# Kernel optimization log

Measured on AMD Instinct MI355X. Metric: run time of the kernel, lower is better.

Reference implementation:

```python
import jax, jax.numpy as jnp
import numpy as np

N = 50_000          # nodes
E = 1_600_000       # edges (avg degree 32)
F_IN = 8            # num_static_node_features
F_OUT = 12          # num_timesteps_in (TGCN hidden)
PERIODS = 6         # num_timesteps_out


def setup_inputs() -> dict:
    key = jax.random.key(0)
    ks = jax.random.split(key, 12)
    def n(k, shape, s=0.2):
        return jax.random.normal(k, shape, jnp.float32) * s
    return {
        "x": jax.random.normal(ks[0], (N, F_IN, PERIODS), jnp.float32),
        "edge_index": jax.random.randint(ks[1], (2, E), 0, N, dtype=jnp.int32),
        "edge_weight": jax.random.uniform(ks[2], (E,), jnp.float32),
        "att": n(ks[3], (PERIODS,), 1.0),
        "Wz": n(ks[4], (F_IN, F_OUT)), "bz": jnp.zeros((F_OUT,), jnp.float32),
        "Wr": n(ks[5], (F_IN, F_OUT)), "br": jnp.zeros((F_OUT,), jnp.float32),
        "Wh": n(ks[6], (F_IN, F_OUT)), "bh": jnp.zeros((F_OUT,), jnp.float32),
        "lzW": n(ks[7], (F_OUT, 2 * F_OUT)), "lzb": jnp.zeros((F_OUT,), jnp.float32),
        "lrW": n(ks[8], (F_OUT, 2 * F_OUT)), "lrb": jnp.zeros((F_OUT,), jnp.float32),
        "lhW": n(ks[9], (F_OUT, 2 * F_OUT)), "lhb": jnp.zeros((F_OUT,), jnp.float32),
        "linW": n(ks[10], (PERIODS, F_OUT)), "linb": jnp.zeros((PERIODS,), jnp.float32),
    }


def _gcn_norm(edge_index, edge_weight):
    # PyG gcn_norm: add self loops (weight 1.0), symmetric D^-1/2 A D^-1/2,
    # degree computed from dst (col) of edge_weight.
    src, dst = edge_index[0], edge_index[1]
    loop = jnp.arange(N, dtype=src.dtype)
    src = jnp.concatenate([src, loop])
    dst = jnp.concatenate([dst, loop])
    ew = jnp.concatenate([edge_weight, jnp.ones((N,), edge_weight.dtype)])
    deg = jax.ops.segment_sum(ew, dst, num_segments=N)
    dinv = jnp.where(deg > 0, 1.0 / jnp.sqrt(deg), 0.0)
    return src, dst, dinv[src] * ew * dinv[dst]


def _gcn_conv(xp, W, b, src, dst, norm):
    h = xp @ W                                  # [N, F_OUT]
    msg = norm[:, None] * h[src]                # gather over edges
    return jax.ops.segment_sum(msg, dst, num_segments=N) + b


def reference(x, edge_index, edge_weight, att, Wz, bz, Wr, br, Wh, bh,
              lzW, lzb, lrW, lrb, lhW, lhb, linW, linb):
    src, dst, norm = _gcn_norm(edge_index, edge_weight)
    H0 = jnp.zeros((N, F_OUT), x.dtype)  # A3TGCN passes H=None each period

    def tgcn_cell(xp):  # xp: [N, F_IN]
        Z = jax.nn.sigmoid(
            jnp.concatenate([_gcn_conv(xp, Wz, bz, src, dst, norm), H0], -1) @ lzW.T + lzb)
        R = jax.nn.sigmoid(
            jnp.concatenate([_gcn_conv(xp, Wr, br, src, dst, norm), H0], -1) @ lrW.T + lrb)
        Ht = jnp.tanh(
            jnp.concatenate([_gcn_conv(xp, Wh, bh, src, dst, norm), H0 * R], -1) @ lhW.T + lhb)
        return Z * H0 + (1.0 - Z) * Ht

    probs = jax.nn.softmax(att)                  # [P]
    Hs = jax.vmap(tgcn_cell, in_axes=2)(x)       # [P, N, F_OUT]
    H = jnp.einsum('p,pnf->nf', probs, Hs)       # attention-weighted sum
    h = jax.nn.relu(H)
    return h @ linW.T + linb                     # [N, PERIODS]
```

## Files before the change

kernel.cpp:

```cpp
#include <hip/hip_runtime.h>
#include <hip/hip_fp16.h>

#define N_NODES 50000
#define N_EDGES 1600000
#define F_IN 8
#define F_OUT 12
#define PERIODS 6
#define FP 48
#define BKT_SH 7
#define BKT_N 128
#define NBKT ((N_NODES + BKT_N - 1) / BKT_N)
#define CHK 2048
#define NCHK ((N_EDGES + CHK - 1) / CHK)
#define SEG_CAP 4736
#define SRC_MASK 0x1FFFFu

__global__ void __launch_bounds__(256) k_hist(const int* __restrict__ dst,
                                              unsigned int* __restrict__ hist) {
    __shared__ unsigned int h[NBKT];
    int tid = threadIdx.x, blk = blockIdx.x;
    for (int k = tid; k < NBKT; k += 256) h[k] = 0u;
    __syncthreads();
    int base = blk * CHK;
    for (int i = tid; i < CHK; i += 256) {
        int e = base + i;
        if (e < N_EDGES) atomicAdd(&h[dst[e] >> BKT_SH], 1u);
    }
    __syncthreads();
    for (int k = tid; k < NBKT; k += 256) hist[(size_t)blk * NBKT + k] = h[k];
}

__global__ void __launch_bounds__(1024) k_colscan(unsigned int* __restrict__ hist,
                                                  unsigned int* __restrict__ tot) {
    __shared__ unsigned int arr[1024];
    int t = threadIdx.x, k = blockIdx.x;
    unsigned int v = (t < NCHK) ? hist[(size_t)t * NBKT + k] : 0u;
    arr[t] = v;
    __syncthreads();
    for (int off = 1; off < 1024; off <<= 1) {
        unsigned int u = (t >= off) ? arr[t - off] : 0u;
        __syncthreads();
        arr[t] += u;
        __syncthreads();
    }
    if (t < NCHK) hist[(size_t)t * NBKT + k] = arr[t] - v;
    if (t == NCHK - 1) tot[k] = arr[t];
}

__global__ void __launch_bounds__(512) k_scatter(const int* __restrict__ src,
                                                 const int* __restrict__ dst,
                                                 const float* __restrict__ ew,
                                                 const unsigned int* __restrict__ colpre,
                                                 const unsigned int* __restrict__ tot,
                                                 unsigned long long* __restrict__ part) {
    __shared__ unsigned int arr[512];
    __shared__ unsigned int ldsOff[NBKT];
    int tid = threadIdx.x, blk = blockIdx.x;
    unsigned int v = (tid < NBKT) ? tot[tid] : 0u;
    arr[tid] = v;
    __syncthreads();
    for (int off = 1; off < 512; off <<= 1) {
        unsigned int u = (tid >= off) ? arr[tid - off] : 0u;
        __syncthreads();
        arr[tid] += u;
        __syncthreads();
    }
    if (tid < NBKT)
        ldsOff[tid] = (arr[tid] - v) + colpre[(size_t)blk * NBKT + tid];
    __syncthreads();
    int base = blk * CHK;
    for (int i = tid; i < CHK; i += 512) {
        int e = base + i;
        if (e >= N_EDGES) continue;
        int s = src[e], d = dst[e];
        unsigned int pos = atomicAdd(&ldsOff[d >> BKT_SH], 1u);
        unsigned int lo = ((unsigned int)(d & (BKT_N - 1)) << 24) | (unsigned int)s;
        part[pos] = ((unsigned long long)__float_as_uint(ew[e]) << 32) | lo;
    }
}

__global__ void __launch_bounds__(512) k_bucket(unsigned long long* __restrict__ part,
                                                const unsigned int* __restrict__ tot,
                                                const float* __restrict__ x,
                                                int* __restrict__ offs,
                                                float* __restrict__ dinv_g,
                                                uint2* __restrict__ xs) {
    __shared__ uint2 stage[SEG_CAP];
    __shared__ unsigned int arr[512];
    __shared__ unsigned int cnt[BKT_N], cnt2[BKT_N], rowstart[BKT_N], sc[BKT_N];
    __shared__ float degf[BKT_N], dinv_l[BKT_N];
    int tid = threadIdx.x, k = blockIdx.x;
    unsigned int v = (tid < NBKT) ? tot[tid] : 0u;
    arr[tid] = v;
    __syncthreads();
    for (int off = 1; off < 512; off <<= 1) {
        unsigned int u = (tid >= off) ? arr[tid - off] : 0u;
        __syncthreads();
        arr[tid] += u;
        __syncthreads();
    }
    unsigned int base = (k > 0) ? arr[k - 1] : 0u;
    unsigned int m = tot[k];
    if (m > SEG_CAP) m = SEG_CAP;
    if (tid < BKT_N) { cnt[tid] = 0u; cnt2[tid] = 0u; degf[tid] = 1.0f; }
    __syncthreads();
    for (unsigned int i = tid; i < m; i += 512) {
        unsigned long long p = part[base + i];
        unsigned int lo = (unsigned int)p;
        unsigned int hi = (unsigned int)(p >> 32);
        stage[i] = make_uint2(lo, hi);
        unsigned int j = (lo >> 24) & (BKT_N - 1);
        atomicAdd(&cnt[j], 1u);
        atomicAdd(&degf[j], __uint_as_float(hi));
    }
    __syncthreads();
    if (tid < BKT_N) sc[tid] = cnt[tid];
    __syncthreads();
    for (int off = 1; off < BKT_N; off <<= 1) {
        unsigned int u = (tid >= (unsigned)off && tid < BKT_N) ? sc[tid - off] : 0u;
        __syncthreads();
        if (tid < BKT_N) sc[tid] += u;
        __syncthreads();
    }
    if (tid < BKT_N) rowstart[tid] = sc[tid] - cnt[tid];
    __syncthreads();

    int n0 = k * BKT_N;
    int nn = N_NODES - n0; if (nn > BKT_N) nn = BKT_N;

    if (tid < BKT_N) {
        float dv = rsqrtf(degf[tid]);
        dinv_l[tid] = dv;
        if (tid < nn) {
            dinv_g[n0 + tid] = dv;
            offs[n0 + tid] = (int)(base + rowstart[tid]);
        }
    }
    if (k == NBKT - 1 && tid == 0) offs[N_NODES] = N_EDGES;

    for (unsigned int i = tid; i < m; i += 512) {
        uint2 vv = stage[i];
        unsigned int j = (vv.x >> 24) & (BKT_N - 1);
        unsigned int r = atomicAdd(&cnt2[j], 1u);
        part[base + rowstart[j] + r] = ((unsigned long long)vv.y << 32) | vv.x;
    }
    __syncthreads();

    for (int idx = tid; idx < nn * 12; idx += 512) {
        int j = idx / 12, c = idx % 12;
        int n = n0 + j;
        float di = dinv_l[j];
        const float4* xr = (const float4*)(x + (size_t)n * FP + c * 4);
        float4 a = xr[0];
        __half2 h0 = __floats2half2_rn(di * a.x, di * a.y);
        __half2 h1 = __floats2half2_rn(di * a.z, di * a.w);
        uint2 o;
        o.x = *(unsigned int*)&h0; o.y = *(unsigned int*)&h1;
        xs[(size_t)n * 12 + c] = o;
    }
}

__global__ void __launch_bounds__(256) k_gather(const uint2* __restrict__ xs,
                                                const float* __restrict__ dinv,
                                                const int* __restrict__ offs,
                                                const unsigned long long* __restrict__ part,
                                                uint2* __restrict__ xagg2) {
    int t = blockIdx.x * 256 + threadIdx.x;
    if (t >= N_NODES * 12) return;
    int n = t / 12, c = t % 12;
    uint2 self = xs[(size_t)n * 12 + c];
    float2 f0 = __half22float2(*(__half2*)&self.x);
    float2 f1 = __half22float2(*(__half2*)&self.y);
    float a0 = f0.x, a1 = f0.y, a2 = f1.x, a3 = f1.y;
    int b = offs[n], e = offs[n + 1];
    int kk = b;
    for (; kk + 8 <= e; kk += 8) {
        unsigned long long p[8];
        uint2 v[8];
        #pragma unroll
        for (int u = 0; u < 8; u++) p[u] = part[kk + u];
        #pragma unroll
        for (int u = 0; u < 8; u++)
            v[u] = xs[(size_t)((unsigned int)p[u] & SRC_MASK) * 12 + c];
        #pragma unroll
        for (int u = 0; u < 8; u++) {
            float w = __uint_as_float((unsigned int)(p[u] >> 32));
            float2 e0 = __half22float2(*(__half2*)&v[u].x);
            float2 e1 = __half22float2(*(__half2*)&v[u].y);
            a0 += w * e0.x; a1 += w * e0.y; a2 += w * e1.x; a3 += w * e1.y;
        }
    }
    for (; kk + 4 <= e; kk += 4) {
        unsigned long long p[4];
        uint2 v[4];
        #pragma unroll
        for (int u = 0; u < 4; u++) p[u] = part[kk + u];
        #pragma unroll
        for (int u = 0; u < 4; u++)
            v[u] = xs[(size_t)((unsigned int)p[u] & SRC_MASK) * 12 + c];
        #pragma unroll
        for (int u = 0; u < 4; u++) {
            float w = __uint_as_float((unsigned int)(p[u] >> 32));
            float2 e0 = __half22float2(*(__half2*)&v[u].x);
            float2 e1 = __half22float2(*(__half2*)&v[u].y);
            a0 += w * e0.x; a1 += w * e0.y; a2 += w * e1.x; a3 += w * e1.y;
        }
    }
    for (; kk < e; kk++) {
        unsigned long long p = part[kk];
        float w = __uint_as_float((unsigned int)(p >> 32));
        uint2 v = xs[(size_t)((unsigned int)p & SRC_MASK) * 12 + c];
        float2 e0 = __half22float2(*(__half2*)&v.x);
        float2 e1 = __half22float2(*(__half2*)&v.y);
        a0 += w * e0.x; a1 += w * e0.y; a2 += w * e1.x; a3 += w * e1.y;
    }
    float di = dinv[n];
    __half2 o0 = __floats2half2_rn(di * a0, di * a1);
    __half2 o1 = __floats2half2_rn(di * a2, di * a3);
    uint2 o;
    o.x = *(unsigned int*)&o0; o.y = *(unsigned int*)&o1;
    xagg2[(size_t)n * 12 + c] = o;
}

__global__ void k_node(const uint2* __restrict__ xagg2, const float* __restrict__ att,
                       const float* __restrict__ Wz, const float* __restrict__ bz,
                       const float* __restrict__ Wh, const float* __restrict__ bh,
                       const float* __restrict__ lzW, const float* __restrict__ lzb,
                       const float* __restrict__ lhW, const float* __restrict__ lhb,
                       const float* __restrict__ linW, const float* __restrict__ linb,
                       float* __restrict__ out) {
    int n = blockIdx.x * blockDim.x + threadIdx.x;
    if (n >= N_NODES) return;

    float a[PERIODS];
    float m = -1e30f;
    #pragma unroll
    for (int p = 0; p < PERIODS; p++) { a[p] = att[p]; m = fmaxf(m, a[p]); }
    float se = 0.f;
    #pragma unroll
    for (int p = 0; p < PERIODS; p++) { a[p] = __expf(a[p] - m); se += a[p]; }
    float inv = 1.f / se;
    #pragma unroll
    for (int p = 0; p < PERIODS; p++) a[p] *= inv;

    float row[FP];
    const uint2* xr = xagg2 + (size_t)n * 12;
    #pragma unroll
    for (int i = 0; i < 12; i++) {
        uint2 v = xr[i];
        float2 f0 = __half22float2(*(__half2*)&v.x);
        float2 f1 = __half22float2(*(__half2*)&v.y);
        row[4 * i] = f0.x; row[4 * i + 1] = f0.y;
        row[4 * i + 2] = f1.x; row[4 * i + 3] = f1.y;
    }

    float H[F_OUT];
    #pragma unroll
    for (int j = 0; j < F_OUT; j++) H[j] = 0.f;

    for (int p = 0; p < PERIODS; p++) {
        float gz[F_OUT], gh[F_OUT];
        #pragma unroll
        for (int j = 0; j < F_OUT; j++) { gz[j] = bz[j]; gh[j] = bh[j]; }
        #pragma unroll
        for (int f = 0; f < F_IN; f++) {
            float xv = row[f * PERIODS + p];
            #pragma unroll
            for (int j = 0; j < F_OUT; j++) {
                gz[j] += xv * Wz[f * F_OUT + j];
                gh[j] += xv * Wh[f * F_OUT + j];
            }
        }
        #pragma unroll
        for (int j = 0; j < F_OUT; j++) {
            float z = lzb[j], t2 = lhb[j];
            #pragma unroll
            for (int kk = 0; kk < F_OUT; kk++) {
                z  += gz[kk] * lzW[j * (2 * F_OUT) + kk];
                t2 += gh[kk] * lhW[j * (2 * F_OUT) + kk];
            }
            float Z = 1.f / (1.f + __expf(-z));
            H[j] += a[p] * (1.f - Z) * tanhf(t2);
        }
    }

    float* op = out + (size_t)n * PERIODS;
    #pragma unroll
    for (int q = 0; q < PERIODS; q++) {
        float acc = linb[q];
        #pragma unroll
        for (int j = 0; j < F_OUT; j++)
            acc += fmaxf(H[j], 0.f) * linW[q * F_OUT + j];
        op[q] = acc;
    }
}

extern "C" void kernel_launch(void* const* d_in, const int* in_sizes, int n_in,
                              void* d_out, int out_size, void* d_ws, size_t ws_size,
                              hipStream_t stream) {
    const float* x    = (const float*)d_in[0];
    const int*   ei   = (const int*)d_in[1];
    const float* ew   = (const float*)d_in[2];
    const float* att  = (const float*)d_in[3];
    const float* Wz   = (const float*)d_in[4];
    const float* bz   = (const float*)d_in[5];
    const float* Wh   = (const float*)d_in[8];
    const float* bh   = (const float*)d_in[9];
    const float* lzW  = (const float*)d_in[10];
    const float* lzb  = (const float*)d_in[11];
    const float* lhW  = (const float*)d_in[14];
    const float* lhb  = (const float*)d_in[15];
    const float* linW = (const float*)d_in[16];
    const float* linb = (const float*)d_in[17];
    float* out = (float*)d_out;

    unsigned long long* part = (unsigned long long*)d_ws;
    uint2* xs = (uint2*)(part + N_EDGES);
    uint2* xagg2 = xs + (size_t)N_NODES * 12;
    unsigned int* hist = (unsigned int*)(xagg2 + (size_t)N_NODES * 12);
    float* dinv = (float*)(hist + (size_t)NCHK * NBKT);
    int*   offs = (int*)(dinv + N_NODES);
    unsigned int* tot = (unsigned int*)(offs + N_NODES + 1);

    const int* srcp = ei;
    const int* dstp = ei + N_EDGES;

    k_hist<<<NCHK, 256, 0, stream>>>(dstp, hist);
    k_colscan<<<NBKT, 1024, 0, stream>>>(hist, tot);
    k_scatter<<<NCHK, 512, 0, stream>>>(srcp, dstp, ew, hist, tot, part);
    k_bucket<<<NBKT, 512, 0, stream>>>(part, tot, x, offs, dinv, xs);
    k_gather<<<(N_NODES * 12 + 255) / 256, 256, 0, stream>>>(xs, dinv, offs, part, xagg2);
    k_node<<<(N_NODES + 255) / 256, 256, 0, stream>>>(xagg2, att, Wz, bz, Wh, bh,
                                                      lzW, lzb, lhW, lhb, linW, linb, out);
}
```

Before: 220.4 us.

## Replace histogram+scan bucketing with fixed-capacity buckets and atomic cursors

Removes the separate histogram and column-scan kernels. Each bucket now gets a fixed SEG_CAP slot region, and k_scatter claims per-block offsets with one global atomicAdd per bucket on a cursor array. Node offsets become int2 (begin, end) pairs because rows are no longer contiguous across buckets. This saves two kernel launches and a pass over dst, but it drops edges if any bucket overflows SEG_CAP and makes edge order within a bucket nondeterministic.

```diff
diff --git a/kernel.cpp b/kernel.cpp
--- a/kernel.cpp
+++ b/kernel.cpp
@@ -15,92 +15,64 @@
 #define SEG_CAP 4736
 #define SRC_MASK 0x1FFFFu
 
-__global__ void __launch_bounds__(256) k_hist(const int* __restrict__ dst,
-                                              unsigned int* __restrict__ hist) {
-    __shared__ unsigned int h[NBKT];
-    int tid = threadIdx.x, blk = blockIdx.x;
-    for (int k = tid; k < NBKT; k += 256) h[k] = 0u;
-    __syncthreads();
-    int base = blk * CHK;
-    for (int i = tid; i < CHK; i += 256) {
-        int e = base + i;
-        if (e < N_EDGES) atomicAdd(&h[dst[e] >> BKT_SH], 1u);
-    }
-    __syncthreads();
-    for (int k = tid; k < NBKT; k += 256) hist[(size_t)blk * NBKT + k] = h[k];
-}
-
-__global__ void __launch_bounds__(1024) k_colscan(unsigned int* __restrict__ hist,
-                                                  unsigned int* __restrict__ tot) {
-    __shared__ unsigned int arr[1024];
-    int t = threadIdx.x, k = blockIdx.x;
-    unsigned int v = (t < NCHK) ? hist[(size_t)t * NBKT + k] : 0u;
-    arr[t] = v;
-    __syncthreads();
-    for (int off = 1; off < 1024; off <<= 1) {
-        unsigned int u = (t >= off) ? arr[t - off] : 0u;
-        __syncthreads();
-        arr[t] += u;
-        __syncthreads();
-    }
-    if (t < NCHK) hist[(size_t)t * NBKT + k] = arr[t] - v;
-    if (t == NCHK - 1) tot[k] = arr[t];
+__global__ void k_zero(unsigned int* __restrict__ cursor) {
+    int i = threadIdx.x;
+    if (i < NBKT) cursor[i] = 0u;
 }
 
 __global__ void __launch_bounds__(512) k_scatter(const int* __restrict__ src,
                                                  const int* __restrict__ dst,
                                                  const float* __restrict__ ew,
-                                                 const unsigned int* __restrict__ colpre,
-                                                 const unsigned int* __restrict__ tot,
+                                                 unsigned int* __restrict__ cursor,
                                                  unsigned long long* __restrict__ part) {
-    __shared__ unsigned int arr[512];
-    __shared__ unsigned int ldsOff[NBKT];
+    __shared__ unsigned int h[NBKT];
+    __shared__ unsigned int gbase[NBKT];
     int tid = threadIdx.x, blk = blockIdx.x;
-    unsigned int v = (tid < NBKT) ? tot[tid] : 0u;
-    arr[tid] = v;
-    __syncthreads();
-    for (int off = 1; off < 512; off <<= 1) {
-        unsigned int u = (tid >= off) ? arr[tid - off] : 0u;
-        __syncthreads();
-        arr[tid] += u;
-        __syncthreads();
-    }
-    if (tid < NBKT)
-        ldsOff[tid] = (arr[tid] - v) + colpre[(size_t)blk * NBKT + tid];
+    for (int k = tid; k < NBKT; k += 512) h[k] = 0u;
     __syncthreads();
     int base = blk * CHK;
-    for (int i = tid; i < CHK; i += 512) {
-        int e = base + i;
-        if (e >= N_EDGES) continue;
-        int s = src[e], d = dst[e];
-        unsigned int pos = atomicAdd(&ldsOff[d >> BKT_SH], 1u);
-        unsigned int lo = ((unsigned int)(d & (BKT_N - 1)) << 24) | (unsigned int)s;
-        part[pos] = ((unsigned long long)__float_as_uint(ew[e]) << 32) | lo;
+    int bv[4]; unsigned int lr[4], lo[4], hiw[4]; bool val[4];
+    #pragma unroll
+    for (int u = 0; u < 4; u++) {
+        int e = base + u * 512 + tid;
+        val[u] = (e < N_EDGES);
+        if (val[u]) {
+            int s = src[e], d = dst[e];
+            int b = d >> BKT_SH;
+            bv[u] = b;
+            lr[u] = atomicAdd(&h[b], 1u);
+            lo[u] = ((unsigned int)(d & (BKT_N - 1)) << 24) | (unsigned int)s;
+            hiw[u] = __float_as_uint(ew[e]);
+        }
+    }
+    __syncthreads();
+    for (int k = tid; k < NBKT; k += 512) {
+        unsigned int c = h[k];
+        gbase[k] = c ? atomicAdd(&cursor[k], c) : 0u;
+    }
+    __syncthreads();
+    #pragma unroll
+    for (int u = 0; u < 4; u++) {
+        if (!val[u]) continue;
+        unsigned int off = gbase[bv[u]] + lr[u];
+        if (off < SEG_CAP)
+            part[(size_t)bv[u] * SEG_CAP + off] =
+                ((unsigned long long)hiw[u] << 32) | lo[u];
     }
 }
 
 __global__ void __launch_bounds__(512) k_bucket(unsigned long long* __restrict__ part,
-                                                const unsigned int* __restrict__ tot,
+                                                const unsigned int* __restrict__ cursor,
                                                 const float* __restrict__ x,
-                                                int* __restrict__ offs,
+                                                int2* __restrict__ offs2,
                                                 float* __restrict__ dinv_g,
                                                 uint2* __restrict__ xs) {
     __shared__ uint2 stage[SEG_CAP];
-    __shared__ unsigned int arr[512];
     __shared__ unsigned int cnt[BKT_N], cnt2[BKT_N], rowstart[BKT_N], sc[BKT_N];
     __shared__ float degf[BKT_N], dinv_l[BKT_N];
     int tid = threadIdx.x, k = blockIdx.x;
-    unsigned int v = (tid < NBKT) ? tot[tid] : 0u;
-    arr[tid] = v;
-    __syncthreads();
-    for (int off = 1; off < 512; off <<= 1) {
-        unsigned int u = (tid >= off) ? arr[tid - off] : 0u;
-        __syncthreads();
-        arr[tid] += u;
-        __syncthreads();
-    }
-    unsigned int base = (k > 0) ? arr[k - 1] : 0u;
-    unsigned int m = tot[k];
+    unsigned int base = (unsigned int)k * SEG_CAP;
+    unsigned int m = cursor[k];
     if (m > SEG_CAP) m = SEG_CAP;
     if (tid < BKT_N) { cnt[tid] = 0u; cnt2[tid] = 0u; degf[tid] = 1.0f; }
     __syncthreads();
@@ -133,10 +105,10 @@
         dinv_l[tid] = dv;
         if (tid < nn) {
             dinv_g[n0 + tid] = dv;
-            offs[n0 + tid] = (int)(base + rowstart[tid]);
-        }
-    }
-    if (k == NBKT - 1 && tid == 0) offs[N_NODES] = N_EDGES;
+            offs2[n0 + tid] = make_int2((int)(base + rowstart[tid]),
+                                        (int)(base + sc[tid]));
+        }
+    }
 
     for (unsigned int i = tid; i < m; i += 512) {
         uint2 vv = stage[i];
@@ -162,7 +134,7 @@
 
 __global__ void __launch_bounds__(256) k_gather(const uint2* __restrict__ xs,
                                                 const float* __restrict__ dinv,
-                                                const int* __restrict__ offs,
+                                                const int2* __restrict__ offs2,
                                                 const unsigned long long* __restrict__ part,
                                                 uint2* __restrict__ xagg2) {
     int t = blockIdx.x * 256 + threadIdx.x;
@@ -172,7 +144,8 @@
     float2 f0 = __half22float2(*(__half2*)&self.x);
     float2 f1 = __half22float2(*(__half2*)&self.y);
     float a0 = f0.x, a1 = f0.y, a2 = f1.x, a3 = f1.y;
-    int b = offs[n], e = offs[n + 1];
+    int2 oe = offs2[n];
+    int b = oe.x, e = oe.y;
     int kk = b;
     for (; kk + 8 <= e; kk += 8) {
         unsigned long long p[8];
@@ -315,21 +288,19 @@
     float* out = (float*)d_out;
 
     unsigned long long* part = (unsigned long long*)d_ws;
-    uint2* xs = (uint2*)(part + N_EDGES);
+    uint2* xs = (uint2*)(part + (size_t)NBKT * SEG_CAP);
     uint2* xagg2 = xs + (size_t)N_NODES * 12;
-    unsigned int* hist = (unsigned int*)(xagg2 + (size_t)N_NODES * 12);
-    float* dinv = (float*)(hist + (size_t)NCHK * NBKT);
-    int*   offs = (int*)(dinv + N_NODES);
-    unsigned int* tot = (unsigned int*)(offs + N_NODES + 1);
+    float* dinv = (float*)(xagg2 + (size_t)N_NODES * 12);
+    int2*  offs2 = (int2*)(dinv + N_NODES);
+    unsigned int* cursor = (unsigned int*)(offs2 + N_NODES);
 
     const int* srcp = ei;
     const int* dstp = ei + N_EDGES;
 
-    k_hist<<<NCHK, 256, 0, stream>>>(dstp, hist);
-    k_colscan<<<NBKT, 1024, 0, stream>>>(hist, tot);
-    k_scatter<<<NCHK, 512, 0, stream>>>(srcp, dstp, ew, hist, tot, part);
-    k_bucket<<<NBKT, 512, 0, stream>>>(part, tot, x, offs, dinv, xs);
-    k_gather<<<(N_NODES * 12 + 255) / 256, 256, 0, stream>>>(xs, dinv, offs, part, xagg2);
+    k_zero<<<1, 512, 0, stream>>>(cursor);
+    k_scatter<<<NCHK, 512, 0, stream>>>(srcp, dstp, ew, cursor, part);
+    k_bucket<<<NBKT, 512, 0, stream>>>(part, cursor, x, offs2, dinv, xs);
+    k_gather<<<(N_NODES * 12 + 255) / 256, 256, 0, stream>>>(xs, dinv, offs2, part, xagg2);
     k_node<<<(N_NODES + 255) / 256, 256, 0, stream>>>(xagg2, att, Wz, bz, Wh, bh,
                                                       lzW, lzb, lhW, lhb, linW, linb, out);
 }
```

After: 217.3 us. About the same (-1.4%).
